# Kernel tuning notes

Measured on AMD Instinct MI355X. Metric: run time of the kernel, lower is better.

## Reference

```python
import jax, jax.numpy as jnp
import numpy as np

B, T, C = 16, 1023, 2048
N_LAYER, LAYER_ID = 24, 12


def setup_inputs() -> dict:
    key = jax.random.key(0)
    k0, k1, k2, k3, k4 = jax.random.split(key, 5)
    x = jax.random.normal(k0, (B, T, C), jnp.float32)
    # decay schedule exactly as in RWKV_TimeMix.__init__ (first_sa_layer_id = 1)
    f1 = 3.0 + (LAYER_ID - 1) / (N_LAYER - 2) * (1.2 - 3.0)
    f2 = 0.65 + (LAYER_ID - 1) / (N_LAYER - 2) * (0.4 - 0.65)
    h = np.arange(C, dtype=np.float64)
    decay_speed = np.power(f2, h / (C - 1) * 7) * f1
    time_decay = jnp.asarray(np.log(decay_speed), jnp.float32)          # [C]
    time_first = jnp.full((C,), float(np.log(0.3)), jnp.float32)        # [C]
    time_mix = jnp.concatenate([jnp.zeros((C // 2,), jnp.float32),
                                jnp.ones((C - C // 2,), jnp.float32)])  # [C]
    s = 0.02
    Wk = jax.random.normal(k1, (C, C), jnp.float32) * s
    Wv = jax.random.normal(k2, (C, C), jnp.float32) * s
    Wr = jax.random.normal(k3, (C, C), jnp.float32) * s
    Wo = jax.random.normal(k4, (C, C), jnp.float32) * s
    z = jnp.zeros((B, C), jnp.float32)
    return {"x": x, "time_decay": time_decay, "time_first": time_first,
            "time_mix": time_mix, "Wk": Wk, "Wv": Wv, "Wr": Wr, "Wo": Wo,
            "xx": z, "aa": z, "bb": z, "mm": z}


def reference(x, time_decay, time_first, time_mix, Wk, Wv, Wr, Wo, xx, aa, bb, mm):
    Bn, Tn, Cn = x.shape
    # time_shift: prepend carried last-token state xx, drop last
    x_shift = jnp.concatenate([xx[:, None, :], x[:, :-1, :]], axis=1)
    xm = x * time_mix + x_shift * (1.0 - time_mix)
    k = xm @ Wk.T                       # [B, T, C]
    v = xm @ Wv.T
    r = xm @ Wr.T
    # running-max renorm to the nearest power of two: ldexp(0.5, frexp(max_t k).exponent)
    kmax = jax.lax.stop_gradient(jnp.max(k, axis=1))   # [B, C], max over time
    _, expo = jnp.frexp(kmax)
    mm_new = jnp.ldexp(jnp.float32(0.5), expo)          # [B, C]
    k = jnp.exp(k - mm_new[:, None, :])
    kv = k * v
    # TimeX kernel weights: w[c, T-1-delta] = exp(-exp(time_decay[c]) * (delta-1)) = d**(delta-1),
    # w[c, T-1] = exp(time_first[c]); so wk[t] = e_first*k[t] + sum_{u<t} d^{t-1-u} k[u] -> linear scan
    d = jnp.exp(-jnp.exp(time_decay))                   # [C] per-channel decay (= w[...,-3])
    e_first = jnp.exp(time_first)                       # [C] (w[...,-1])
    rsf = jnp.exp(mm - mm_new)                          # rescale carried state to new renorm
    k_seq = jnp.concatenate([(bb * rsf)[:, None, :], k], axis=1)    # [B, T+1, C]
    kv_seq = jnp.concatenate([(aa * rsf)[:, None, :], kv], axis=1)  # [B, T+1, C]

    def step(carry, inp):
        Sk, Skv = carry
        kt, kvt = inp
        out = (e_first * kt + Sk, e_first * kvt + Skv)
        return (d * Sk + kt, d * Skv + kvt), out

    init = (jnp.zeros((Bn, Cn), x.dtype), jnp.zeros((Bn, Cn), x.dtype))
    seq = (jnp.swapaxes(k_seq, 0, 1), jnp.swapaxes(kv_seq, 0, 1))   # [T+1, B, C]
    _, (wk_s, wkv_s) = jax.lax.scan(step, init, seq)
    wk = jnp.swapaxes(wk_s[1:], 0, 1)     # drop state slot -> [B, T, C]
    wkv = jnp.swapaxes(wkv_s[1:], 0, 1)
    rwkv = jax.nn.sigmoid(r) * jnp.nan_to_num(wkv / wk)
    return rwkv @ Wo.T
```

## Files before the change

### kernel.cpp

```cpp
#include <hip/hip_runtime.h>
#include <hip/hip_bf16.h>
#include <hip/hip_fp16.h>
#include <math.h>
#include <float.h>

#define BB 16
#define TT 1023
#define CC 2048
#define M_ROWS (BB * TT)
#define MP 16384
#define N3 (3 * CC)
#define NCH 16
#define CHL 64

typedef __attribute__((ext_vector_type(8))) short bfrag;
typedef __attribute__((ext_vector_type(4))) float f32x4;
typedef __attribute__((ext_vector_type(4))) short short4v;

__device__ __forceinline__ void async16(const void* g, void* l) {
  __builtin_amdgcn_global_load_lds((const __attribute__((address_space(1))) void*)g,
                                   (__attribute__((address_space(3))) void*)l, 16, 0, 0);
}

__device__ __forceinline__ short bfb(float f) {
  __hip_bfloat16 h = __float2bfloat16(f);
  return *reinterpret_cast<short*>(&h);
}

__global__ void cast_weights(const float* __restrict__ Wk, const float* __restrict__ Wv,
                             const float* __restrict__ Wr, const float* __restrict__ Wo,
                             __hip_bfloat16* __restrict__ W3, __hip_bfloat16* __restrict__ WoB) {
  size_t i4 = (size_t)blockIdx.x * 256 + threadIdx.x;
  size_t i = i4 * 4;
  float4 a = *(const float4*)(Wk + i);
  float4 b = *(const float4*)(Wv + i);
  float4 c = *(const float4*)(Wr + i);
  float4 d = *(const float4*)(Wo + i);
  *(short4v*)((short*)W3 + i)              = short4v{bfb(a.x), bfb(a.y), bfb(a.z), bfb(a.w)};
  *(short4v*)((short*)W3 + i + CC * CC)    = short4v{bfb(b.x), bfb(b.y), bfb(b.z), bfb(b.w)};
  *(short4v*)((short*)W3 + i + 2 * CC * CC) = short4v{bfb(c.x), bfb(c.y), bfb(c.z), bfb(c.w)};
  *(short4v*)((short*)WoB + i)             = short4v{bfb(d.x), bfb(d.y), bfb(d.z), bfb(d.w)};
}

__global__ void build_xm(const float* __restrict__ x, const float* __restrict__ xx,
                         const float* __restrict__ tmix, __hip_bfloat16* __restrict__ xm) {
  int m = blockIdx.x;
  short* orow = (short*)xm + (size_t)m * CC;
  if (m >= M_ROWS) {
    for (int c = threadIdx.x; c < CC / 4; c += 256)
      ((short4v*)orow)[c] = short4v{0, 0, 0, 0};
    return;
  }
  int b = m / TT, t = m - b * TT;
  const float* xrow = x + (size_t)m * CC;
  const float* xprev = (t == 0) ? (xx + (size_t)b * CC) : (xrow - CC);
  for (int c = threadIdx.x; c < CC / 4; c += 256) {
    float4 xv = ((const float4*)xrow)[c];
    float4 pv = ((const float4*)xprev)[c];
    float4 tm = ((const float4*)tmix)[c];
    ((short4v*)orow)[c] = short4v{
        bfb(xv.x * tm.x + pv.x * (1.0f - tm.x)),
        bfb(xv.y * tm.y + pv.y * (1.0f - tm.y)),
        bfb(xv.z * tm.z + pv.z * (1.0f - tm.z)),
        bfb(xv.w * tm.w + pv.w * (1.0f - tm.w))};
  }
}

template <int MODE>
__global__ __launch_bounds__(512, 2)
void gemm256(const short* __restrict__ A, const short* __restrict__ Bw,
             float* __restrict__ outF, __half* __restrict__ outH,
             __hip_bfloat16* __restrict__ outV, __hip_bfloat16* __restrict__ outR) {
  __shared__ short lds[65536];

  const int lane = threadIdx.x & 63, wid = threadIdx.x >> 6;
  const int wr = wid >> 2, wc = wid & 3;

  const int nx = gridDim.x;
  const int nwg = nx * gridDim.y;
  const int bid = blockIdx.y * nx + blockIdx.x;
  const int q = nwg >> 3;
  const int swz = (bid & 7) * q + (bid >> 3);
  const int mBase = (swz / nx) * 256;
  const int nBase = (swz % nx) * 256;

  const int srow = lane >> 2;
  const int scol = (((lane & 3) ^ ((lane >> 3) & 3)) * 8);
  const int stgOff = wid * 1024 + lane * 8;
  const short* aSrcBase = A  + (size_t)(mBase + wid * 32 + srow) * CC + scol;
  const short* bSrcBase = Bw + (size_t)(nBase + wid * 32 + srow) * CC + scol;

  const int ldOff = (lane & 15) * 32 + (((lane >> 4) ^ ((lane >> 1) & 3)) * 8);

  f32x4 acc[2][4][4] = {};
  bfrag bq[4];

#define RGNA(buf, kh) ((buf) * 32768 + (kh) * 8192)
#define RGNB(buf, kh) (16384 + (buf) * 32768 + (kh) * 8192)

#define STG_A(buf, kh, tk) do { \
    const short* _s = aSrcBase + ((tk) * 64 + (kh) * 32); \
    short* _d = lds + RGNA(buf, kh) + stgOff; \
    async16(_s, _d); async16(_s + (size_t)16 * CC, _d + 512); } while (0)

#define STG_B(buf, kh, tk) do { \
    const short* _s = bSrcBase + ((tk) * 64 + (kh) * 32); \
    short* _d = lds + RGNB(buf, kh) + stgOff; \
    async16(_s, _d); async16(_s + (size_t)16 * CC, _d + 512); } while (0)

#define VMN(n) asm volatile("s_waitcnt vmcnt(" #n ")" ::: "memory")

#define PH(buf, kh, mh, STAGE, WAIT) do { \
    bfrag aq[4]; \
    if ((mh) == 0) { \
      _Pragma("unroll") \
      for (int n = 0; n < 4; ++n) \
        bq[n] = *(const bfrag*)(lds + RGNB(buf, kh) + (wc * 64 + n * 16) * 32 + ldOff); \
    } \
    _Pragma("unroll") \
    for (int f = 0; f < 4; ++f) \
      aq[f] = *(const bfrag*)(lds + RGNA(buf, kh) + (wr * 128 + (mh) * 64 + f * 16) * 32 + ldOff); \
    STAGE; \
    __builtin_amdgcn_s_setprio(1); \
    _Pragma("unroll") \
    for (int f = 0; f < 4; ++f) \
      _Pragma("unroll") \
      for (int n = 0; n < 4; ++n) \
        acc[mh][f][n] = __builtin_amdgcn_mfma_f32_16x16x32_bf16(aq[f], bq[n], acc[mh][f][n], 0, 0, 0); \
    __builtin_amdgcn_s_setprio(0); \
    WAIT; \
    __builtin_amdgcn_s_barrier(); } while (0)

  STG_A(0, 0, 0); STG_B(0, 0, 0);
  STG_A(0, 1, 0); STG_B(0, 1, 0);
  STG_A(1, 0, 1); STG_B(1, 0, 1);
  VMN(4);
  __builtin_amdgcn_s_barrier();

  for (int ti = 0; ti < 30; ti += 2) {
    PH(0, 0, 0, STG_A(1, 1, ti + 1), );
    PH(0, 0, 1, STG_B(1, 1, ti + 1), );
    PH(0, 1, 0, STG_A(0, 0, ti + 2), );
    PH(0, 1, 1, STG_B(0, 0, ti + 2), VMN(4));
    PH(1, 0, 0, STG_A(0, 1, ti + 2), );
    PH(1, 0, 1, STG_B(0, 1, ti + 2), );
    PH(1, 1, 0, STG_A(1, 0, ti + 3), );
    PH(1, 1, 1, STG_B(1, 0, ti + 3), VMN(4));
  }
  PH(0, 0, 0, STG_A(1, 1, 31), );
  PH(0, 0, 1, STG_B(1, 1, 31), );
  PH(0, 1, 0, , );
  PH(0, 1, 1, , VMN(4));
  PH(1, 0, 0, , );
  PH(1, 0, 1, , VMN(0));
  PH(1, 1, 0, , );
  PH(1, 1, 1, , );

#undef PH
#undef VMN
#undef STG_A
#undef STG_B
#undef RGNA
#undef RGNB

#pragma unroll
  for (int mh = 0; mh < 2; ++mh)
#pragma unroll
    for (int f = 0; f < 4; ++f) {
      const int row0 = mBase + wr * 128 + mh * 64 + f * 16 + (lane >> 4) * 4;
      const int col0 = nBase + wc * 64 + (lane & 15);
#pragma unroll
      for (int n = 0; n < 4; ++n) {
        const int col = col0 + n * 16;
#pragma unroll
        for (int rr = 0; rr < 4; ++rr) {
          const int row = row0 + rr;
          if (row < M_ROWS) {
            float val = acc[mh][f][n][rr];
            if constexpr (MODE == 0) {
              outF[(size_t)row * CC + col] = val;
            } else {
              if (col < CC)          outH[(size_t)row * CC + col] = __float2half(expf(val));
              else if (col < 2 * CC) outV[(size_t)row * CC + (col - CC)] = __float2bfloat16(val);
              else                   outR[(size_t)row * CC + (col - 2 * CC)] = __float2bfloat16(val);
            }
          }
        }
      }
    }
}

__global__ __launch_bounds__(1024)
void scan_fuse2(const __half* __restrict__ ek, const __hip_bfloat16* __restrict__ v,
                const __hip_bfloat16* __restrict__ r, const float* __restrict__ aa,
                const float* __restrict__ bb, const float* __restrict__ mm,
                const float* __restrict__ tdec, const float* __restrict__ tfir,
                __hip_bfloat16* __restrict__ rwkv) {
  __shared__ float sBk[NCH][64], sBkv[NCH][64], sSk[NCH][64], sSkv[NCH][64];

  const int lane = threadIdx.x & 63, wid = threadIdx.x >> 6;
  const int c = blockIdx.x * 64 + lane;
  const int b = blockIdx.y;
  const int i = b * CC + c;

  const float dexp = expf(tdec[c]);
  const float d    = expf(-dexp);
  const float ef   = expf(tfir[c]);

  const int t0 = wid * CHL;
  const int t1 = (t0 + CHL < TT) ? t0 + CHL : TT;
  const size_t base = (size_t)b * TT * CC + c;

  if (wid < NCH - 1) {
    float Bk = 0.0f, Bkv = 0.0f;
    size_t off = base + (size_t)t0 * CC;
#pragma unroll 4
    for (int t = t0; t < t1; ++t, off += CC) {
      float kk = __half2float(ek[off]);
      float kv = kk * __bfloat162float(v[off]);
      Bk = d * Bk + kk;
      Bkv = d * Bkv + kv;
    }
    sBk[wid][lane] = Bk;
    sBkv[wid][lane] = Bkv;
  }
  __syncthreads();

  if (wid == 0) {
    const float d64 = expf(-dexp * (float)CHL);
    const float sc = expf(mm[i]);
    float S = bb[i] * sc, Sv = aa[i] * sc;
#pragma unroll
    for (int j = 0; j < NCH; ++j) {
      sSk[j][lane] = S;
      sSkv[j][lane] = Sv;
      if (j < NCH - 1) {
        S = d64 * S + sBk[j][lane];
        Sv = d64 * Sv + sBkv[j][lane];
      }
    }
  }
  __syncthreads();

  float S = sSk[wid][lane], Sv = sSkv[wid][lane];
  size_t off = base + (size_t)t0 * CC;
#pragma unroll 4
  for (int t = t0; t < t1; ++t, off += CC) {
    float kk = __half2float(ek[off]);
    float vv = __bfloat162float(v[off]);
    float rv = __bfloat162float(r[off]);
    float kv = kk * vv;
    float wk = ef * kk + S;
    float wkv = ef * kv + Sv;
    S = d * S + kk;
    Sv = d * Sv + kv;
    float ratio = wkv / wk;
    if (isnan(ratio)) ratio = 0.0f;
    else if (isinf(ratio)) ratio = ratio > 0.0f ? FLT_MAX : -FLT_MAX;
    float sig = 1.0f / (1.0f + expf(-rv));
    rwkv[off] = __float2bfloat16(sig * ratio);
  }
}

extern "C" void kernel_launch(void* const* d_in, const int* in_sizes, int n_in,
                              void* d_out, int out_size, void* d_ws, size_t ws_size,
                              hipStream_t stream) {
  const float* x    = (const float*)d_in[0];
  const float* tdec = (const float*)d_in[1];
  const float* tfir = (const float*)d_in[2];
  const float* tmix = (const float*)d_in[3];
  const float* Wk   = (const float*)d_in[4];
  const float* Wv   = (const float*)d_in[5];
  const float* Wr   = (const float*)d_in[6];
  const float* Wo   = (const float*)d_in[7];
  const float* xx   = (const float*)d_in[8];
  const float* aa   = (const float*)d_in[9];
  const float* bb   = (const float*)d_in[10];
  const float* mm   = (const float*)d_in[11];

  char* ws = (char*)d_ws;
  size_t o = 0;
  __hip_bfloat16* W3  = (__hip_bfloat16*)(ws + o); o += (size_t)N3 * CC * 2;
  __hip_bfloat16* WoB = (__hip_bfloat16*)(ws + o); o += (size_t)CC * CC * 2;
  __hip_bfloat16* xmB = (__hip_bfloat16*)(ws + o); o += (size_t)MP * CC * 2;
  __hip_bfloat16* vB  = (__hip_bfloat16*)(ws + o); o += (size_t)MP * CC * 2;
  __hip_bfloat16* rB  = (__hip_bfloat16*)(ws + o); o += (size_t)MP * CC * 2;

  __half* ekH = (__half*)d_out;
  __hip_bfloat16* rwkvB = xmB;

  cast_weights<<<CC * CC / 1024, 256, 0, stream>>>(Wk, Wv, Wr, Wo, W3, WoB);
  build_xm<<<MP, 256, 0, stream>>>(x, xx, tmix, xmB);
  gemm256<1><<<dim3(N3 / 256, MP / 256), 512, 0, stream>>>(
      (const short*)xmB, (const short*)W3, nullptr, ekH, vB, rB);
  scan_fuse2<<<dim3(CC / 64, BB), 1024, 0, stream>>>(ekH, vB, rB, aa, bb, mm,
                                                     tdec, tfir, rwkvB);
  gemm256<0><<<dim3(CC / 256, MP / 256), 512, 0, stream>>>(
      (const short*)rwkvB, (const short*)WoB, (float*)d_out, nullptr, nullptr, nullptr);
}
```

Measured before the change: 674.0 us.

## Merge prep kernels, move sigmoid into GEMM epilogue, reorder tile swizzle

Combines the weight cast and xm build into one prep launch, which saves a kernel launch and lets both run concurrently. The sigmoid of r now runs in the first GEMM epilogue instead of in the scan loop, shortening the latency-bound scan. The GEMM tile mapping walks M fastest instead of N, which changes which tiles share weights or activations in cache. Applying sigmoid before the bf16 rounding slightly changes numerics.

```diff
diff --git a/kernel.cpp b/kernel.cpp
--- a/kernel.cpp
+++ b/kernel.cpp
@@ -27,42 +27,45 @@
   return *reinterpret_cast<short*>(&h);
 }
 
-__global__ void cast_weights(const float* __restrict__ Wk, const float* __restrict__ Wv,
-                             const float* __restrict__ Wr, const float* __restrict__ Wo,
-                             __hip_bfloat16* __restrict__ W3, __hip_bfloat16* __restrict__ WoB) {
-  size_t i4 = (size_t)blockIdx.x * 256 + threadIdx.x;
-  size_t i = i4 * 4;
-  float4 a = *(const float4*)(Wk + i);
-  float4 b = *(const float4*)(Wv + i);
-  float4 c = *(const float4*)(Wr + i);
-  float4 d = *(const float4*)(Wo + i);
-  *(short4v*)((short*)W3 + i)              = short4v{bfb(a.x), bfb(a.y), bfb(a.z), bfb(a.w)};
-  *(short4v*)((short*)W3 + i + CC * CC)    = short4v{bfb(b.x), bfb(b.y), bfb(b.z), bfb(b.w)};
-  *(short4v*)((short*)W3 + i + 2 * CC * CC) = short4v{bfb(c.x), bfb(c.y), bfb(c.z), bfb(c.w)};
-  *(short4v*)((short*)WoB + i)             = short4v{bfb(d.x), bfb(d.y), bfb(d.z), bfb(d.w)};
-}
-
-__global__ void build_xm(const float* __restrict__ x, const float* __restrict__ xx,
-                         const float* __restrict__ tmix, __hip_bfloat16* __restrict__ xm) {
-  int m = blockIdx.x;
-  short* orow = (short*)xm + (size_t)m * CC;
-  if (m >= M_ROWS) {
-    for (int c = threadIdx.x; c < CC / 4; c += 256)
-      ((short4v*)orow)[c] = short4v{0, 0, 0, 0};
-    return;
-  }
-  int b = m / TT, t = m - b * TT;
-  const float* xrow = x + (size_t)m * CC;
-  const float* xprev = (t == 0) ? (xx + (size_t)b * CC) : (xrow - CC);
-  for (int c = threadIdx.x; c < CC / 4; c += 256) {
-    float4 xv = ((const float4*)xrow)[c];
-    float4 pv = ((const float4*)xprev)[c];
-    float4 tm = ((const float4*)tmix)[c];
-    ((short4v*)orow)[c] = short4v{
-        bfb(xv.x * tm.x + pv.x * (1.0f - tm.x)),
-        bfb(xv.y * tm.y + pv.y * (1.0f - tm.y)),
-        bfb(xv.z * tm.z + pv.z * (1.0f - tm.z)),
-        bfb(xv.w * tm.w + pv.w * (1.0f - tm.w))};
+__global__ void prep(const float* __restrict__ x, const float* __restrict__ xx,
+                     const float* __restrict__ tmix,
+                     const float* __restrict__ Wk, const float* __restrict__ Wv,
+                     const float* __restrict__ Wr, const float* __restrict__ Wo,
+                     __hip_bfloat16* __restrict__ xm,
+                     __hip_bfloat16* __restrict__ W3, __hip_bfloat16* __restrict__ WoB) {
+  int bid = blockIdx.x;
+  if (bid < MP) {
+    int m = bid;
+    short* orow = (short*)xm + (size_t)m * CC;
+    if (m >= M_ROWS) {
+      for (int c = threadIdx.x; c < CC / 4; c += 256)
+        ((short4v*)orow)[c] = short4v{0, 0, 0, 0};
+      return;
+    }
+    int b = m / TT, t = m - b * TT;
+    const float* xrow = x + (size_t)m * CC;
+    const float* xprev = (t == 0) ? (xx + (size_t)b * CC) : (xrow - CC);
+    for (int c = threadIdx.x; c < CC / 4; c += 256) {
+      float4 xv = ((const float4*)xrow)[c];
+      float4 pv = ((const float4*)xprev)[c];
+      float4 tm = ((const float4*)tmix)[c];
+      ((short4v*)orow)[c] = short4v{
+          bfb(xv.x * tm.x + pv.x * (1.0f - tm.x)),
+          bfb(xv.y * tm.y + pv.y * (1.0f - tm.y)),
+          bfb(xv.z * tm.z + pv.z * (1.0f - tm.z)),
+          bfb(xv.w * tm.w + pv.w * (1.0f - tm.w))};
+    }
+  } else {
+    size_t i4 = (size_t)(bid - MP) * 256 + threadIdx.x;
+    size_t i = i4 * 4;
+    float4 a = *(const float4*)(Wk + i);
+    float4 b = *(const float4*)(Wv + i);
+    float4 c = *(const float4*)(Wr + i);
+    float4 d = *(const float4*)(Wo + i);
+    *(short4v*)((short*)W3 + i)               = short4v{bfb(a.x), bfb(a.y), bfb(a.z), bfb(a.w)};
+    *(short4v*)((short*)W3 + i + CC * CC)     = short4v{bfb(b.x), bfb(b.y), bfb(b.z), bfb(b.w)};
+    *(short4v*)((short*)W3 + i + 2 * CC * CC) = short4v{bfb(c.x), bfb(c.y), bfb(c.z), bfb(c.w)};
+    *(short4v*)((short*)WoB + i)              = short4v{bfb(d.x), bfb(d.y), bfb(d.z), bfb(d.w)};
   }
 }
 
@@ -76,13 +79,13 @@
   const int lane = threadIdx.x & 63, wid = threadIdx.x >> 6;
   const int wr = wid >> 2, wc = wid & 3;
 
-  const int nx = gridDim.x;
-  const int nwg = nx * gridDim.y;
+  const int nx = gridDim.x, ny = gridDim.y;
+  const int nwg = nx * ny;
   const int bid = blockIdx.y * nx + blockIdx.x;
   const int q = nwg >> 3;
   const int swz = (bid & 7) * q + (bid >> 3);
-  const int mBase = (swz / nx) * 256;
-  const int nBase = (swz % nx) * 256;
+  const int mBase = (swz % ny) * 256;
+  const int nBase = (swz / ny) * 256;
 
   const int srow = lane >> 2;
   const int scol = (((lane & 3) ^ ((lane >> 3) & 3)) * 8);
@@ -182,7 +185,8 @@
             } else {
               if (col < CC)          outH[(size_t)row * CC + col] = __float2half(expf(val));
               else if (col < 2 * CC) outV[(size_t)row * CC + (col - CC)] = __float2bfloat16(val);
-              else                   outR[(size_t)row * CC + (col - 2 * CC)] = __float2bfloat16(val);
+              else                   outR[(size_t)row * CC + (col - 2 * CC)] =
+                                         __float2bfloat16(1.0f / (1.0f + expf(-val)));
             }
           }
         }
@@ -192,7 +196,7 @@
 
 __global__ __launch_bounds__(1024)
 void scan_fuse2(const __half* __restrict__ ek, const __hip_bfloat16* __restrict__ v,
-                const __hip_bfloat16* __restrict__ r, const float* __restrict__ aa,
+                const __hip_bfloat16* __restrict__ sg, const float* __restrict__ aa,
                 const float* __restrict__ bb, const float* __restrict__ mm,
                 const float* __restrict__ tdec, const float* __restrict__ tfir,
                 __hip_bfloat16* __restrict__ rwkv) {
@@ -248,7 +252,7 @@
   for (int t = t0; t < t1; ++t, off += CC) {
     float kk = __half2float(ek[off]);
     float vv = __bfloat162float(v[off]);
-    float rv = __bfloat162float(r[off]);
+    float sig = __bfloat162float(sg[off]);
     float kv = kk * vv;
     float wk = ef * kk + S;
     float wkv = ef * kv + Sv;
@@ -257,7 +261,6 @@
     float ratio = wkv / wk;
     if (isnan(ratio)) ratio = 0.0f;
     else if (isinf(ratio)) ratio = ratio > 0.0f ? FLT_MAX : -FLT_MAX;
-    float sig = 1.0f / (1.0f + expf(-rv));
     rwkv[off] = __float2bfloat16(sig * ratio);
   }
 }
@@ -284,16 +287,16 @@
   __hip_bfloat16* WoB = (__hip_bfloat16*)(ws + o); o += (size_t)CC * CC * 2;
   __hip_bfloat16* xmB = (__hip_bfloat16*)(ws + o); o += (size_t)MP * CC * 2;
   __hip_bfloat16* vB  = (__hip_bfloat16*)(ws + o); o += (size_t)MP * CC * 2;
-  __hip_bfloat16* rB  = (__hip_bfloat16*)(ws + o); o += (size_t)MP * CC * 2;
+  __hip_bfloat16* sgB = (__hip_bfloat16*)(ws + o); o += (size_t)MP * CC * 2;
 
   __half* ekH = (__half*)d_out;
   __hip_bfloat16* rwkvB = xmB;
 
-  cast_weights<<<CC * CC / 1024, 256, 0, stream>>>(Wk, Wv, Wr, Wo, W3, WoB);
-  build_xm<<<MP, 256, 0, stream>>>(x, xx, tmix, xmB);
+  prep<<<MP + CC * CC / 1024, 256, 0, stream>>>(x, xx, tmix, Wk, Wv, Wr, Wo,
+                                                xmB, W3, WoB);
   gemm256<1><<<dim3(N3 / 256, MP / 256), 512, 0, stream>>>(
-      (const short*)xmB, (const short*)W3, nullptr, ekH, vB, rB);
-  scan_fuse2<<<dim3(CC / 64, BB), 1024, 0, stream>>>(ekH, vB, rB, aa, bb, mm,
+      (const short*)xmB, (const short*)W3, nullptr, ekH, vB, sgB);
+  scan_fuse2<<<dim3(CC / 64, BB), 1024, 0, stream>>>(ekH, vB, sgB, aa, bb, mm,
                                                      tdec, tfir, rwkvB);
   gemm256<0><<<dim3(CC / 256, MP / 256), 512, 0, stream>>>(
       (const short*)rwkvB, (const short*)WoB, (float*)d_out, nullptr, nullptr, nullptr);
```

Result: slower. 749.0 us (+11.1%).
